# Kernel optimization log

Measured on AMD Instinct MI355X. Metric: run time of the kernel, lower is better.

## Reference

```python
import jax, jax.numpy as jnp
import numpy as np

B, C, H, W = 32, 256, 56, 56
RED = 4  # reduction


def setup_inputs() -> dict:
    key = jax.random.key(0)
    k_x, k_w1, k_b1, k_w2, k_b2 = jax.random.split(key, 5)
    cr = C // RED
    return {
        "x": jax.random.normal(k_x, (B, C, H, W), dtype=jnp.float32),
        # condition[1]: Conv2d(C, C//r, 1) acting on 1x1 maps == linear
        "w1": jax.random.normal(k_w1, (cr, C), dtype=jnp.float32) * 0.02,
        "b1": jax.random.normal(k_b1, (cr,), dtype=jnp.float32) * 0.02,
        # condition[3]: Conv2d(C//r, 9*C, 1)
        "w2": jax.random.normal(k_w2, (9 * C, cr), dtype=jnp.float32) * 0.02,
        "b2": jax.random.normal(k_b2, (9 * C,), dtype=jnp.float32) * 0.02,
    }


def reference(x, w1, b1, w2, b2):
    b, c, h, w = x.shape
    # global average pool -> [B, C]
    gap = jnp.mean(x, axis=(2, 3))
    # 1x1 conv on 1x1 spatial == dense layer; exact (erf) GELU like nn.GELU()
    hid = jax.nn.gelu(gap @ w1.T + b1, approximate=False)  # [B, C//r]
    logits = hid @ w2.T + b2  # [B, 9*C]
    # softmax over the 9 kernel taps per (b, c)
    wk = jax.nn.softmax(logits.reshape(b, c, 9), axis=2)
    kern = wk.reshape(b * c, 1, 3, 3)  # OIHW, one output ch per group
    # per-(batch,channel) dynamic 3x3 depthwise conv via huge-group grouped conv
    y = jax.lax.conv_general_dilated(
        x.reshape(1, b * c, h, w),
        kern,
        window_strides=(1, 1),
        padding=((1, 1), (1, 1)),
        dimension_numbers=("NCHW", "OIHW", "NCHW"),
        feature_group_count=b * c,
    )
    return y.reshape(b, c, h, w) + x
```

## Files before the change

### kernel.cpp

```cpp
#include <hip/hip_runtime.h>
#include <math.h>

#define B_  32
#define C_  256
#define H_  56
#define W_  56
#define CR_ 64
#define HW_ (H_*W_)
#define BC_ (B_*C_)

__global__ __launch_bounds__(256) void gap_kernel(const float* __restrict__ x,
                                                  float* __restrict__ gap) {
    const int bc = blockIdx.x;
    const float4* p4 = (const float4*)(x + (size_t)bc * HW_);
    float s = 0.f;
    for (int i = threadIdx.x; i < HW_ / 4; i += 256) {
        float4 v = p4[i];
        s += (v.x + v.y) + (v.z + v.w);
    }
    for (int off = 32; off > 0; off >>= 1) s += __shfl_down(s, off, 64);
    __shared__ float ws[4];
    const int lane = threadIdx.x & 63, wid = threadIdx.x >> 6;
    if (lane == 0) ws[wid] = s;
    __syncthreads();
    if (threadIdx.x == 0) {
        float t = (ws[0] + ws[1]) + (ws[2] + ws[3]);
        gap[bc] = t * (1.0f / (float)HW_);
    }
}

__global__ __launch_bounds__(256) void hid_kernel(const float* __restrict__ gap,
                                                  const float* __restrict__ w1,
                                                  const float* __restrict__ b1,
                                                  float* __restrict__ hid_g) {
    const int b = blockIdx.x;
    const int j = threadIdx.x >> 2;
    const int part = threadIdx.x & 3;
    const float4* wr = (const float4*)(w1 + (size_t)j * C_) + part * 16;
    const float4* gv = (const float4*)(gap + (size_t)b * C_) + part * 16;
    float acc = 0.f;
    #pragma unroll
    for (int q = 0; q < 16; ++q) {
        float4 w = wr[q], g = gv[q];
        acc += w.x * g.x + w.y * g.y + w.z * g.z + w.w * g.w;
    }
    acc += __shfl_xor(acc, 1, 64);
    acc += __shfl_xor(acc, 2, 64);
    if (part == 0) {
        acc += b1[j];
        hid_g[b * CR_ + j] = 0.5f * acc * (1.0f + erff(acc * 0.7071067811865476f));
    }
}

__global__ __launch_bounds__(256) void dconv_kernel(const float* __restrict__ x,
                                                    const float* __restrict__ hid_g,
                                                    const float* __restrict__ w2,
                                                    const float* __restrict__ b2,
                                                    float* __restrict__ out) {
    const int bc = blockIdx.x;
    const int b  = bc >> 8;
    const int c  = bc & 255;
    const float* p = x + (size_t)bc * HW_;
    float* o = out + (size_t)bc * HW_;

    __shared__ float sm[58 * 64];
    __shared__ float lgs[9];
    float4* sm4 = (float4*)sm;

    const int tid = threadIdx.x;

    if (tid < 116) {
        const int r = (tid & 1) ? 57 : 0;
        sm[r * 64 + 3 + (tid >> 1)] = 0.f;
    } else if (tid < 228) {
        const int i = tid - 116;
        sm[(1 + (i >> 1)) * 64 + ((i & 1) ? 60 : 3)] = 0.f;
    }

    if (tid < 9) {
        const float4* wr = (const float4*)(w2 + ((size_t)c * 9 + tid) * CR_);
        const float4* hv = (const float4*)(hid_g + (size_t)b * CR_);
        float acc = b2[c * 9 + tid];
        #pragma unroll
        for (int q = 0; q < 16; ++q) {
            float4 w = wr[q], h = hv[q];
            acc += w.x * h.x + w.y * h.y + w.z * h.z + w.w * h.w;
        }
        lgs[tid] = acc;
    }

    const float4* p4 = (const float4*)p;
    for (int i = tid; i < HW_ / 4; i += 256) {
        const int y = i / 14, q = i - y * 14;
        sm4[(y + 1) * 16 + 1 + q] = p4[i];
    }
    __syncthreads();

    float l0 = lgs[0], l1 = lgs[1], l2 = lgs[2], l3 = lgs[3], l4 = lgs[4],
          l5 = lgs[5], l6 = lgs[6], l7 = lgs[7], l8 = lgs[8];
    float mx = fmaxf(fmaxf(fmaxf(fmaxf(l0, l1), fmaxf(l2, l3)),
                           fmaxf(fmaxf(l4, l5), fmaxf(l6, l7))), l8);
    float k0 = __expf(l0 - mx), k1 = __expf(l1 - mx), k2 = __expf(l2 - mx),
          k3 = __expf(l3 - mx), k4 = __expf(l4 - mx), k5 = __expf(l5 - mx),
          k6 = __expf(l6 - mx), k7 = __expf(l7 - mx), k8 = __expf(l8 - mx);
    const float inv = 1.0f / (((k0 + k1) + (k2 + k3)) + ((k4 + k5) + (k6 + k7)) + k8);
    k0 *= inv; k1 *= inv; k2 *= inv; k3 *= inv; k4 *= inv;
    k5 *= inv; k6 *= inv; k7 *= inv; k8 *= inv;

    const int xc = tid & 63;
    const int g  = tid >> 6;
    if (xc < 56) {
        const int y0 = g * 14;
        const float* base = sm + xc + 3;
        const float* r0 = base + (y0) * 64;
        const float* r1 = base + (y0 + 1) * 64;
        float a0 = r0[0], a1 = r0[1], a2 = r0[2];
        float b0 = r1[0], b1 = r1[1], b2 = r1[2];
        #pragma unroll
        for (int r = 0; r < 14; ++r) {
            const float* r2 = base + (y0 + 2 + r) * 64;
            const float c0 = r2[0], c1 = r2[1], c2 = r2[2];
            const float v = a0 * k0 + a1 * k1 + a2 * k2
                          + b0 * k3 + b1 * k4 + b2 * k5
                          + c0 * k6 + c1 * k7 + c2 * k8
                          + b1;
            o[(y0 + r) * W_ + xc] = v;
            a0 = b0; a1 = b1; a2 = b2;
            b0 = c0; b1 = c1; b2 = c2;
        }
    }
}

extern "C" void kernel_launch(void* const* d_in, const int* in_sizes, int n_in,
                              void* d_out, int out_size, void* d_ws, size_t ws_size,
                              hipStream_t stream) {
    const float* x  = (const float*)d_in[0];
    const float* w1 = (const float*)d_in[1];
    const float* b1 = (const float*)d_in[2];
    const float* w2 = (const float*)d_in[3];
    const float* b2 = (const float*)d_in[4];
    float* out = (float*)d_out;

    float* gap   = (float*)d_ws;
    float* hid_g = gap + BC_;

    gap_kernel<<<BC_, 256, 0, stream>>>(x, gap);
    hid_kernel<<<B_, 256, 0, stream>>>(gap, w1, b1, hid_g);
    dconv_kernel<<<BC_, 256, 0, stream>>>(x, hid_g, w2, b2, out);
}
```

Measured before the change: 61.30 us.

## Compute four outputs per thread with float4 LDS reads and 128-thread blocks

```diff
diff --git a/kernel.cpp b/kernel.cpp
--- a/kernel.cpp
+++ b/kernel.cpp
@@ -8,6 +8,9 @@
 #define CR_ 64
 #define HW_ (H_*W_)
 #define BC_ (B_*C_)
+
+#define SMS  68
+#define SMS4 17
 
 __global__ __launch_bounds__(256) void gap_kernel(const float* __restrict__ x,
                                                   float* __restrict__ gap) {
@@ -52,7 +55,7 @@
     }
 }
 
-__global__ __launch_bounds__(256) void dconv_kernel(const float* __restrict__ x,
+__global__ __launch_bounds__(128) void dconv_kernel(const float* __restrict__ x,
                                                     const float* __restrict__ hid_g,
                                                     const float* __restrict__ w2,
                                                     const float* __restrict__ b2,
@@ -63,18 +66,17 @@
     const float* p = x + (size_t)bc * HW_;
     float* o = out + (size_t)bc * HW_;
 
-    __shared__ float sm[58 * 64];
+    __shared__ float sm[58 * SMS];
     __shared__ float lgs[9];
     float4* sm4 = (float4*)sm;
-
     const int tid = threadIdx.x;
 
-    if (tid < 116) {
+    if (tid < 34) {
         const int r = (tid & 1) ? 57 : 0;
-        sm[r * 64 + 3 + (tid >> 1)] = 0.f;
-    } else if (tid < 228) {
-        const int i = tid - 116;
-        sm[(1 + (i >> 1)) * 64 + ((i & 1) ? 60 : 3)] = 0.f;
+        sm4[r * SMS4 + (tid >> 1)] = make_float4(0.f, 0.f, 0.f, 0.f);
+    }
+    if (tid < 112) {
+        sm[(1 + (tid >> 1)) * SMS + ((tid & 1) ? 60 : 3)] = 0.f;
     }
 
     if (tid < 9) {
@@ -90,9 +92,9 @@
     }
 
     const float4* p4 = (const float4*)p;
-    for (int i = tid; i < HW_ / 4; i += 256) {
+    for (int i = tid; i < HW_ / 4; i += 128) {
         const int y = i / 14, q = i - y * 14;
-        sm4[(y + 1) * 16 + 1 + q] = p4[i];
+        sm4[(y + 1) * SMS4 + 1 + q] = p4[i];
     }
     __syncthreads();
 
@@ -107,26 +109,41 @@
     k0 *= inv; k1 *= inv; k2 *= inv; k3 *= inv; k4 *= inv;
     k5 *= inv; k6 *= inv; k7 *= inv; k8 *= inv;
 
-    const int xc = tid & 63;
-    const int g  = tid >> 6;
-    if (xc < 56) {
-        const int y0 = g * 14;
-        const float* base = sm + xc + 3;
-        const float* r0 = base + (y0) * 64;
-        const float* r1 = base + (y0 + 1) * 64;
-        float a0 = r0[0], a1 = r0[1], a2 = r0[2];
-        float b0 = r1[0], b1 = r1[1], b2 = r1[2];
+    if (tid < 112) {
+        const int s  = tid / 14;
+        const int cg = tid - s * 14;
+        const int y0 = s * 7;
+        const float* base = sm + y0 * SMS + 4 + 4 * cg;
+
+        float4 A  = *(const float4*)(base);
+        float La = base[-1], Ra = base[4];
+        const float* r1 = base + SMS;
+        float4 Bv = *(const float4*)(r1);
+        float Lb = r1[-1], Rb = r1[4];
+
         #pragma unroll
-        for (int r = 0; r < 14; ++r) {
-            const float* r2 = base + (y0 + 2 + r) * 64;
-            const float c0 = r2[0], c1 = r2[1], c2 = r2[2];
-            const float v = a0 * k0 + a1 * k1 + a2 * k2
-                          + b0 * k3 + b1 * k4 + b2 * k5
-                          + c0 * k6 + c1 * k7 + c2 * k8
-                          + b1;
-            o[(y0 + r) * W_ + xc] = v;
-            a0 = b0; a1 = b1; a2 = b2;
-            b0 = c0; b1 = c1; b2 = c2;
+        for (int r = 0; r < 7; ++r) {
+            const float* r2 = base + (r + 2) * SMS;
+            const float4 Cv = *(const float4*)(r2);
+            const float Lc = r2[-1], Rc = r2[4];
+
+            const float o0 = La  * k0 + A.x * k1 + A.y * k2
+                           + Lb  * k3 + Bv.x * k4 + Bv.y * k5
+                           + Lc  * k6 + Cv.x * k7 + Cv.y * k8 + Bv.x;
+            const float o1 = A.x * k0 + A.y * k1 + A.z * k2
+                           + Bv.x * k3 + Bv.y * k4 + Bv.z * k5
+                           + Cv.x * k6 + Cv.y * k7 + Cv.z * k8 + Bv.y;
+            const float o2 = A.y * k0 + A.z * k1 + A.w * k2
+                           + Bv.y * k3 + Bv.z * k4 + Bv.w * k5
+                           + Cv.y * k6 + Cv.z * k7 + Cv.w * k8 + Bv.z;
+            const float o3 = A.z * k0 + A.w * k1 + Ra  * k2
+                           + Bv.z * k3 + Bv.w * k4 + Rb  * k5
+                           + Cv.z * k6 + Cv.w * k7 + Rc  * k8 + Bv.w;
+
+            *(float4*)(o + (y0 + r) * W_ + 4 * cg) = make_float4(o0, o1, o2, o3);
+
+            A = Bv; La = Lb; Ra = Rb;
+            Bv = Cv; Lb = Lc; Rb = Rc;
         }
     }
 }
@@ -146,5 +163,5 @@
 
     gap_kernel<<<BC_, 256, 0, stream>>>(x, gap);
     hid_kernel<<<B_, 256, 0, stream>>>(gap, w1, b1, hid_g);
-    dconv_kernel<<<BC_, 256, 0, stream>>>(x, hid_g, w2, b2, out);
+    dconv_kernel<<<BC_, 128, 0, stream>>>(x, hid_g, w2, b2, out);
 }
```

After: 66.10 us. 7.8% more time.
